# Kernel tuning notes

Hardware: AMD Instinct MI355X
Metric: run time of the kernel (lower is better)

Reference implementation:

```python
import jax, jax.numpy as jnp
import numpy as np

# module hyperparameters (from init_kwargs): kernel_size=(KH,KW), stride_size=(SH,SW)
KH, KW = 8, 8
SH, SW = 4, 4


def setup_inputs() -> dict:
    key = jax.random.key(0)
    x = jax.random.normal(key, (8, 64, 96, 96), dtype=jnp.float32)
    return {"x": x}


def _local_autocorr(x):
    """Local window self-correlation.

    For each kH x kW window (extracted with stride (SH,SW)), compute the
    correlation of the window with itself shifted by every offset
    (dy - KH//2, dx - KW//2), dy in [0,KH), dx in [0,KW), zero-padded
    outside the window. Output: [B, C, nH, nW, KH, KW].
    """
    B, C, H, W = x.shape
    nH = (H - KH) // SH + 1
    nW = (W - KW) // SW + 1
    # window gather indices
    ys = (jnp.arange(nH) * SH)[:, None] + jnp.arange(KH)[None, :]  # [nH, KH]
    xs = (jnp.arange(nW) * SW)[:, None] + jnp.arange(KW)[None, :]  # [nW, KW]
    # [B, C, nH, KH, nW, KW] -> [N, KH, KW], N = B*C*nH*nW
    patches = x[:, :, ys[:, :, None, None], xs[None, None, :, :]]
    patches = patches.transpose(0, 1, 2, 4, 3, 5).reshape(-1, KH, KW)
    N = patches.shape[0]
    # zero-pad each window so every shift stays in-bounds
    pt, pb = KH // 2, KH - 1 - KH // 2
    pl, pr = KW // 2, KW - 1 - KW // 2
    padded = jnp.pad(patches, ((0, 0), (pt, pb), (pl, pr)))  # [N, 2KH-1, 2KW-1]
    # depthwise (per-window) cross-correlation: out[n, dy, dx] =
    #   sum_{y,x} padded[n, dy + y, dx + x] * patches[n, y, x]
    out = jax.lax.conv_general_dilated(
        padded[None],           # [1, N, 2KH-1, 2KW-1]
        patches[:, None],       # [N, 1, KH, KW]
        window_strides=(1, 1),
        padding='VALID',
        dimension_numbers=('NCHW', 'OIHW', 'NCHW'),
        feature_group_count=N,
    )[0]                        # [N, KH, KW]
    return out.reshape(B, C, nH, nW, KH, KW)


def reference(x):
    return _local_autocorr(x)
```

## Files before the change

### kernel.cpp

```cpp
#include <hip/hip_runtime.h>


constexpr int KH = 8, KW = 8, SH = 4, SW = 4;
constexpr int B = 8, C = 64, H = 96, W = 96;
constexpr int nH = (H - KH) / SH + 1;
constexpr int nW = (W - KW) / SW + 1;
constexpr int NWIN = B * C * nH * nW;
constexpr int TPB = 256;
constexpr int WPB = 128;
constexpr int OSTRIDE = 65;

__global__ __launch_bounds__(TPB) void
local_autocorr_kernel(const float* __restrict__ x, float* __restrict__ out) {
    __shared__ float lds[64 * OSTRIDE];

    const int tid  = threadIdx.x;
    const int role = tid >> 7;
    const int k    = tid & 127;
    const int n    = blockIdx.x * WPB + k;

    const int w  = n % nW;
    const int tt = n / nW;
    const int h  = tt % nH;
    const int bc = tt / nH;

    const float* xp = x + ((size_t)bc * H + (size_t)h * SH) * W + (size_t)w * SW;

    float acc4[8], acc3[8], acc2[8], acc1[8], acc0[8];
    float c50 = 0.f, c60 = 0.f, c70 = 0.f;

    if (role == 0) {
#pragma unroll
        for (int dx = 0; dx < 8; ++dx) { acc4[dx] = 0.f; acc3[dx] = 0.f; }
        float rows[8][8];
#pragma unroll
        for (int r = 0; r < 8; ++r) {
            const float4 lo = *reinterpret_cast<const float4*>(xp + (size_t)r * W);
            const float4 hi = *reinterpret_cast<const float4*>(xp + (size_t)r * W + 4);
            rows[r][0]=lo.x; rows[r][1]=lo.y; rows[r][2]=lo.z; rows[r][3]=lo.w;
            rows[r][4]=hi.x; rows[r][5]=hi.y; rows[r][6]=hi.z; rows[r][7]=hi.w;

#pragma unroll
            for (int dx = 0; dx < 8; ++dx) {
                const int OX = dx - 4;
#pragma unroll
                for (int j = 0; j < 8; ++j) {
                    if (j + OX < 0 || j + OX >= 8) continue;
                    acc4[dx] = fmaf(rows[r][j + OX], rows[r][j], acc4[dx]);
                }
            }
            if (r >= 1) {
#pragma unroll
                for (int dx = 0; dx < 8; ++dx) {
                    const int OX = dx - 4;
#pragma unroll
                    for (int j = 0; j < 8; ++j) {
                        if (j + OX < 0 || j + OX >= 8) continue;
                        acc3[dx] = fmaf(rows[r - 1][j + OX], rows[r][j], acc3[dx]);
                    }
                }
                c50 = fmaf(rows[r][0], rows[r - 1][4], c50);
                c50 = fmaf(rows[r][1], rows[r - 1][5], c50);
                c50 = fmaf(rows[r][2], rows[r - 1][6], c50);
                c50 = fmaf(rows[r][3], rows[r - 1][7], c50);
            }
            __builtin_amdgcn_sched_barrier(0);
        }
    } else {
#pragma unroll
        for (int dx = 0; dx < 8; ++dx) { acc2[dx] = 0.f; acc1[dx] = 0.f; acc0[dx] = 0.f; }
        float rows[8][8];
#pragma unroll
        for (int r = 0; r < 8; ++r) {
            const float4 lo = *reinterpret_cast<const float4*>(xp + (size_t)r * W);
            const float4 hi = *reinterpret_cast<const float4*>(xp + (size_t)r * W + 4);
            rows[r][0]=lo.x; rows[r][1]=lo.y; rows[r][2]=lo.z; rows[r][3]=lo.w;
            rows[r][4]=hi.x; rows[r][5]=hi.y; rows[r][6]=hi.z; rows[r][7]=hi.w;

            if (r >= 2) {
#pragma unroll
                for (int dx = 0; dx < 8; ++dx) {
                    const int OX = dx - 4;
#pragma unroll
                    for (int j = 0; j < 8; ++j) {
                        if (j + OX < 0 || j + OX >= 8) continue;
                        acc2[dx] = fmaf(rows[r - 2][j + OX], rows[r][j], acc2[dx]);
                    }
                }
                c60 = fmaf(rows[r][0], rows[r - 2][4], c60);
                c60 = fmaf(rows[r][1], rows[r - 2][5], c60);
                c60 = fmaf(rows[r][2], rows[r - 2][6], c60);
                c60 = fmaf(rows[r][3], rows[r - 2][7], c60);
            }
            if (r >= 3) {
#pragma unroll
                for (int dx = 0; dx < 8; ++dx) {
                    const int OX = dx - 4;
#pragma unroll
                    for (int j = 0; j < 8; ++j) {
                        if (j + OX < 0 || j + OX >= 8) continue;
                        acc1[dx] = fmaf(rows[r - 3][j + OX], rows[r][j], acc1[dx]);
                    }
                }
                c70 = fmaf(rows[r][0], rows[r - 3][4], c70);
                c70 = fmaf(rows[r][1], rows[r - 3][5], c70);
                c70 = fmaf(rows[r][2], rows[r - 3][6], c70);
                c70 = fmaf(rows[r][3], rows[r - 3][7], c70);
            }
            if (r >= 4) {
#pragma unroll
                for (int dx = 0; dx < 8; ++dx) {
                    const int OX = dx - 4;
#pragma unroll
                    for (int j = 0; j < 8; ++j) {
                        if (j + OX < 0 || j + OX >= 8) continue;
                        acc0[dx] = fmaf(rows[r - 4][j + OX], rows[r][j], acc0[dx]);
                    }
                }
            }
            __builtin_amdgcn_sched_barrier(0);
        }
    }

    float* obase = out + (size_t)blockIdx.x * WPB * 64;
#pragma unroll
    for (int p = 0; p < 2; ++p) {
        if ((k >> 6) == p) {
            float* slot = &lds[(k & 63) * OSTRIDE];
            if (role == 0) {
                *reinterpret_cast<float4*>(slot + 24) = make_float4(acc3[0], acc3[1], acc3[2], acc3[3]);
                *reinterpret_cast<float4*>(slot + 28) = make_float4(acc3[4], acc3[5], acc3[6], acc3[7]);
                *reinterpret_cast<float4*>(slot + 32) = make_float4(acc4[0], acc4[1], acc4[2], acc4[3]);
                *reinterpret_cast<float4*>(slot + 36) = make_float4(acc4[4], acc4[5], acc4[6], acc4[7]);
                *reinterpret_cast<float4*>(slot + 40) = make_float4(c50,     acc3[7], acc3[6], acc3[5]);
                *reinterpret_cast<float4*>(slot + 44) = make_float4(acc3[4], acc3[3], acc3[2], acc3[1]);
            } else {
                *reinterpret_cast<float4*>(slot + 0)  = make_float4(acc0[0], acc0[1], acc0[2], acc0[3]);
                *reinterpret_cast<float4*>(slot + 4)  = make_float4(acc0[4], acc0[5], acc0[6], acc0[7]);
                *reinterpret_cast<float4*>(slot + 8)  = make_float4(acc1[0], acc1[1], acc1[2], acc1[3]);
                *reinterpret_cast<float4*>(slot + 12) = make_float4(acc1[4], acc1[5], acc1[6], acc1[7]);
                *reinterpret_cast<float4*>(slot + 16) = make_float4(acc2[0], acc2[1], acc2[2], acc2[3]);
                *reinterpret_cast<float4*>(slot + 20) = make_float4(acc2[4], acc2[5], acc2[6], acc2[7]);
                *reinterpret_cast<float4*>(slot + 48) = make_float4(c60,     acc2[7], acc2[6], acc2[5]);
                *reinterpret_cast<float4*>(slot + 52) = make_float4(acc2[4], acc2[3], acc2[2], acc2[1]);
                *reinterpret_cast<float4*>(slot + 56) = make_float4(c70,     acc1[7], acc1[6], acc1[5]);
                *reinterpret_cast<float4*>(slot + 60) = make_float4(acc1[4], acc1[3], acc1[2], acc1[1]);
            }
        }
        __syncthreads();
#pragma unroll
        for (int kk = 0; kk < 4; ++kk) {
            const int flat4 = tid + kk * TPB;
            const float4 v = *reinterpret_cast<const float4*>(
                &lds[(flat4 >> 4) * OSTRIDE + (flat4 & 15) * 4]);
            *reinterpret_cast<float4*>(obase + (size_t)p * 64 * 64 + flat4 * 4) = v;
        }
        __syncthreads();
    }
}

extern "C" void kernel_launch(void* const* d_in, const int* in_sizes, int n_in,
                              void* d_out, int out_size, void* d_ws, size_t ws_size,
                              hipStream_t stream) {
    const float* x = (const float*)d_in[0];
    float* out = (float*)d_out;

    const int blocks = NWIN / WPB;
    local_autocorr_kernel<<<blocks, TPB, 0, stream>>>(x, out);
}
```

Before: 33.77 us.

## Shrink blocks, remap blocks across XCDs, prefetch rows, single-pass LDS store

Halves the block to 128 threads handling 64 windows, so the LDS staging needs one pass and one barrier instead of two passes with four barriers. Block indices are remapped so consecutive window groups land on the same XCD, which should improve L2 locality of the overlapping input windows. Row loads are issued two rows ahead of the FMA work to hide global latency. The trade-offs are more blocks to schedule and extra register pressure from the prefetch, bounded by the new launch-bounds occupancy hint.

```diff
diff --git a/kernel.cpp b/kernel.cpp
--- a/kernel.cpp
+++ b/kernel.cpp
@@ -6,18 +6,24 @@
 constexpr int nH = (H - KH) / SH + 1;
 constexpr int nW = (W - KW) / SW + 1;
 constexpr int NWIN = B * C * nH * nW;
-constexpr int TPB = 256;
-constexpr int WPB = 128;
+constexpr int TPB = 128;
+constexpr int WPB = 64;
 constexpr int OSTRIDE = 65;
+constexpr int NBLK = NWIN / WPB;
+constexpr int NXCD = 8;
+constexpr int CPX = NBLK / NXCD;
 
-__global__ __launch_bounds__(TPB) void
+__global__ __launch_bounds__(TPB, 2) void
 local_autocorr_kernel(const float* __restrict__ x, float* __restrict__ out) {
-    __shared__ float lds[64 * OSTRIDE];
+    __shared__ float lds[WPB * OSTRIDE];
 
     const int tid  = threadIdx.x;
-    const int role = tid >> 7;
-    const int k    = tid & 127;
-    const int n    = blockIdx.x * WPB + k;
+    const int role = tid >> 6;
+    const int k    = tid & 63;
+
+    const int bid = (int)blockIdx.x;
+    const int blk = (bid % NXCD) * CPX + bid / NXCD;
+    const int n = blk * WPB + k;
 
     const int w  = n % nW;
     const int tt = n / nW;
@@ -26,27 +32,35 @@
 
     const float* xp = x + ((size_t)bc * H + (size_t)h * SH) * W + (size_t)w * SW;
 
-    float acc4[8], acc3[8], acc2[8], acc1[8], acc0[8];
-    float c50 = 0.f, c60 = 0.f, c70 = 0.f;
+#define LOADROW(dst, ri)                                                              \
+    {                                                                                 \
+        const float4 lo_ = *reinterpret_cast<const float4*>(xp + (size_t)(ri)*W);     \
+        const float4 hi_ = *reinterpret_cast<const float4*>(xp + (size_t)(ri)*W + 4); \
+        dst[0]=lo_.x; dst[1]=lo_.y; dst[2]=lo_.z; dst[3]=lo_.w;                       \
+        dst[4]=hi_.x; dst[5]=hi_.y; dst[6]=hi_.z; dst[7]=hi_.w;                       \
+    }
+
+    float* slot = &lds[k * OSTRIDE];
 
     if (role == 0) {
+        float accD0[8], accD1[8];
+        float c50 = 0.f;
 #pragma unroll
-        for (int dx = 0; dx < 8; ++dx) { acc4[dx] = 0.f; acc3[dx] = 0.f; }
+        for (int dx = 0; dx < 8; ++dx) { accD0[dx] = 0.f; accD1[dx] = 0.f; }
+
         float rows[8][8];
+        LOADROW(rows[0], 0)
+        LOADROW(rows[1], 1)
 #pragma unroll
         for (int r = 0; r < 8; ++r) {
-            const float4 lo = *reinterpret_cast<const float4*>(xp + (size_t)r * W);
-            const float4 hi = *reinterpret_cast<const float4*>(xp + (size_t)r * W + 4);
-            rows[r][0]=lo.x; rows[r][1]=lo.y; rows[r][2]=lo.z; rows[r][3]=lo.w;
-            rows[r][4]=hi.x; rows[r][5]=hi.y; rows[r][6]=hi.z; rows[r][7]=hi.w;
-
+            if (r < 6) LOADROW(rows[r + 2], r + 2)
 #pragma unroll
             for (int dx = 0; dx < 8; ++dx) {
                 const int OX = dx - 4;
 #pragma unroll
                 for (int j = 0; j < 8; ++j) {
                     if (j + OX < 0 || j + OX >= 8) continue;
-                    acc4[dx] = fmaf(rows[r][j + OX], rows[r][j], acc4[dx]);
+                    accD0[dx] = fmaf(rows[r][j + OX], rows[r][j], accD0[dx]);
                 }
             }
             if (r >= 1) {
@@ -56,7 +70,7 @@
 #pragma unroll
                     for (int j = 0; j < 8; ++j) {
                         if (j + OX < 0 || j + OX >= 8) continue;
-                        acc3[dx] = fmaf(rows[r - 1][j + OX], rows[r][j], acc3[dx]);
+                        accD1[dx] = fmaf(rows[r - 1][j + OX], rows[r][j], accD1[dx]);
                     }
                 }
                 c50 = fmaf(rows[r][0], rows[r - 1][4], c50);
@@ -66,32 +80,38 @@
             }
             __builtin_amdgcn_sched_barrier(0);
         }
+
+        *reinterpret_cast<float4*>(slot + 24) = make_float4(accD1[0], accD1[1], accD1[2], accD1[3]);
+        *reinterpret_cast<float4*>(slot + 28) = make_float4(accD1[4], accD1[5], accD1[6], accD1[7]);
+        *reinterpret_cast<float4*>(slot + 32) = make_float4(accD0[0], accD0[1], accD0[2], accD0[3]);
+        *reinterpret_cast<float4*>(slot + 36) = make_float4(accD0[4], accD0[5], accD0[6], accD0[7]);
+        *reinterpret_cast<float4*>(slot + 40) = make_float4(c50,      accD1[7], accD1[6], accD1[5]);
+        *reinterpret_cast<float4*>(slot + 44) = make_float4(accD1[4], accD1[3], accD1[2], accD1[1]);
     } else {
+        float accD2[8], accD3[8], accD4[8];
+        float c60 = 0.f, c70 = 0.f;
 #pragma unroll
-        for (int dx = 0; dx < 8; ++dx) { acc2[dx] = 0.f; acc1[dx] = 0.f; acc0[dx] = 0.f; }
+        for (int dx = 0; dx < 8; ++dx) { accD2[dx] = 0.f; accD3[dx] = 0.f; accD4[dx] = 0.f; }
+
         float rows[8][8];
 #pragma unroll
-        for (int r = 0; r < 8; ++r) {
-            const float4 lo = *reinterpret_cast<const float4*>(xp + (size_t)r * W);
-            const float4 hi = *reinterpret_cast<const float4*>(xp + (size_t)r * W + 4);
-            rows[r][0]=lo.x; rows[r][1]=lo.y; rows[r][2]=lo.z; rows[r][3]=lo.w;
-            rows[r][4]=hi.x; rows[r][5]=hi.y; rows[r][6]=hi.z; rows[r][7]=hi.w;
-
-            if (r >= 2) {
+        for (int kk = 0; kk < 4; ++kk) LOADROW(rows[kk], kk)
 #pragma unroll
-                for (int dx = 0; dx < 8; ++dx) {
-                    const int OX = dx - 4;
+        for (int r = 2; r < 8; ++r) {
+            if (r < 6) LOADROW(rows[r + 2], r + 2)
 #pragma unroll
-                    for (int j = 0; j < 8; ++j) {
-                        if (j + OX < 0 || j + OX >= 8) continue;
-                        acc2[dx] = fmaf(rows[r - 2][j + OX], rows[r][j], acc2[dx]);
-                    }
+            for (int dx = 0; dx < 8; ++dx) {
+                const int OX = dx - 4;
+#pragma unroll
+                for (int j = 0; j < 8; ++j) {
+                    if (j + OX < 0 || j + OX >= 8) continue;
+                    accD2[dx] = fmaf(rows[r - 2][j + OX], rows[r][j], accD2[dx]);
                 }
-                c60 = fmaf(rows[r][0], rows[r - 2][4], c60);
-                c60 = fmaf(rows[r][1], rows[r - 2][5], c60);
-                c60 = fmaf(rows[r][2], rows[r - 2][6], c60);
-                c60 = fmaf(rows[r][3], rows[r - 2][7], c60);
             }
+            c60 = fmaf(rows[r][0], rows[r - 2][4], c60);
+            c60 = fmaf(rows[r][1], rows[r - 2][5], c60);
+            c60 = fmaf(rows[r][2], rows[r - 2][6], c60);
+            c60 = fmaf(rows[r][3], rows[r - 2][7], c60);
             if (r >= 3) {
 #pragma unroll
                 for (int dx = 0; dx < 8; ++dx) {
@@ -99,7 +119,7 @@
 #pragma unroll
                     for (int j = 0; j < 8; ++j) {
                         if (j + OX < 0 || j + OX >= 8) continue;
-                        acc1[dx] = fmaf(rows[r - 3][j + OX], rows[r][j], acc1[dx]);
+                        accD3[dx] = fmaf(rows[r - 3][j + OX], rows[r][j], accD3[dx]);
                     }
                 }
                 c70 = fmaf(rows[r][0], rows[r - 3][4], c70);
@@ -114,48 +134,35 @@
 #pragma unroll
                     for (int j = 0; j < 8; ++j) {
                         if (j + OX < 0 || j + OX >= 8) continue;
-                        acc0[dx] = fmaf(rows[r - 4][j + OX], rows[r][j], acc0[dx]);
+                        accD4[dx] = fmaf(rows[r - 4][j + OX], rows[r][j], accD4[dx]);
                     }
                 }
             }
             __builtin_amdgcn_sched_barrier(0);
         }
+
+        *reinterpret_cast<float4*>(slot + 0)  = make_float4(accD4[0], accD4[1], accD4[2], accD4[3]);
+        *reinterpret_cast<float4*>(slot + 4)  = make_float4(accD4[4], accD4[5], accD4[6], accD4[7]);
+        *reinterpret_cast<float4*>(slot + 8)  = make_float4(accD3[0], accD3[1], accD3[2], accD3[3]);
+        *reinterpret_cast<float4*>(slot + 12) = make_float4(accD3[4], accD3[5], accD3[6], accD3[7]);
+        *reinterpret_cast<float4*>(slot + 16) = make_float4(accD2[0], accD2[1], accD2[2], accD2[3]);
+        *reinterpret_cast<float4*>(slot + 20) = make_float4(accD2[4], accD2[5], accD2[6], accD2[7]);
+        *reinterpret_cast<float4*>(slot + 48) = make_float4(c60,      accD2[7], accD2[6], accD2[5]);
+        *reinterpret_cast<float4*>(slot + 52) = make_float4(accD2[4], accD2[3], accD2[2], accD2[1]);
+        *reinterpret_cast<float4*>(slot + 56) = make_float4(c70,      accD3[7], accD3[6], accD3[5]);
+        *reinterpret_cast<float4*>(slot + 60) = make_float4(accD3[4], accD3[3], accD3[2], accD3[1]);
     }
+#undef LOADROW
 
-    float* obase = out + (size_t)blockIdx.x * WPB * 64;
+    __syncthreads();
+
+    float* obase = out + (size_t)blk * WPB * 64;
 #pragma unroll
-    for (int p = 0; p < 2; ++p) {
-        if ((k >> 6) == p) {
-            float* slot = &lds[(k & 63) * OSTRIDE];
-            if (role == 0) {
-                *reinterpret_cast<float4*>(slot + 24) = make_float4(acc3[0], acc3[1], acc3[2], acc3[3]);
-                *reinterpret_cast<float4*>(slot + 28) = make_float4(acc3[4], acc3[5], acc3[6], acc3[7]);
-                *reinterpret_cast<float4*>(slot + 32) = make_float4(acc4[0], acc4[1], acc4[2], acc4[3]);
-                *reinterpret_cast<float4*>(slot + 36) = make_float4(acc4[4], acc4[5], acc4[6], acc4[7]);
-                *reinterpret_cast<float4*>(slot + 40) = make_float4(c50,     acc3[7], acc3[6], acc3[5]);
-                *reinterpret_cast<float4*>(slot + 44) = make_float4(acc3[4], acc3[3], acc3[2], acc3[1]);
-            } else {
-                *reinterpret_cast<float4*>(slot + 0)  = make_float4(acc0[0], acc0[1], acc0[2], acc0[3]);
-                *reinterpret_cast<float4*>(slot + 4)  = make_float4(acc0[4], acc0[5], acc0[6], acc0[7]);
-                *reinterpret_cast<float4*>(slot + 8)  = make_float4(acc1[0], acc1[1], acc1[2], acc1[3]);
-                *reinterpret_cast<float4*>(slot + 12) = make_float4(acc1[4], acc1[5], acc1[6], acc1[7]);
-                *reinterpret_cast<float4*>(slot + 16) = make_float4(acc2[0], acc2[1], acc2[2], acc2[3]);
-                *reinterpret_cast<float4*>(slot + 20) = make_float4(acc2[4], acc2[5], acc2[6], acc2[7]);
-                *reinterpret_cast<float4*>(slot + 48) = make_float4(c60,     acc2[7], acc2[6], acc2[5]);
-                *reinterpret_cast<float4*>(slot + 52) = make_float4(acc2[4], acc2[3], acc2[2], acc2[1]);
-                *reinterpret_cast<float4*>(slot + 56) = make_float4(c70,     acc1[7], acc1[6], acc1[5]);
-                *reinterpret_cast<float4*>(slot + 60) = make_float4(acc1[4], acc1[3], acc1[2], acc1[1]);
-            }
-        }
-        __syncthreads();
-#pragma unroll
-        for (int kk = 0; kk < 4; ++kk) {
-            const int flat4 = tid + kk * TPB;
-            const float4 v = *reinterpret_cast<const float4*>(
-                &lds[(flat4 >> 4) * OSTRIDE + (flat4 & 15) * 4]);
-            *reinterpret_cast<float4*>(obase + (size_t)p * 64 * 64 + flat4 * 4) = v;
-        }
-        __syncthreads();
+    for (int kk = 0; kk < 8; ++kk) {
+        const int flat4 = tid + kk * TPB;
+        const float4 v = *reinterpret_cast<const float4*>(
+            &lds[(flat4 >> 4) * OSTRIDE + (flat4 & 15) * 4]);
+        *reinterpret_cast<float4*>(obase + (size_t)flat4 * 4) = v;
     }
 }
 
@@ -165,6 +172,5 @@
     const float* x = (const float*)d_in[0];
     float* out = (float*)d_out;
 
-    const int blocks = NWIN / WPB;
-    local_autocorr_kernel<<<blocks, TPB, 0, stream>>>(x, out);
+    local_autocorr_kernel<<<NBLK, TPB, 0, stream>>>(x, out);
 }
```

New measurement: 29.56 us. 12.5% less time.
